# Performance work log

Hardware: AMD Instinct MI355X
Metric: run time of the kernel (lower is better)

## Reference

```python
import jax, jax.numpy as jnp
import numpy as np

N_NODES = 50000
N_EDGES = 800000
IN_DIM = 512
HEADS = 4
HID = 64
OUT = 64
NEG_SLOPE = 0.2  # DGL GATConv default


def gat_layer(x, W, attn_l, attn_r, bias, src, dst, n_nodes, heads, d_out):
    # x: [N, F_in], W: [F_in, heads*d_out], attn_l/attn_r: [heads, d_out], bias: [heads, d_out]
    f = (x @ W).reshape(n_nodes, heads, d_out)          # [N, H, D]
    el = jnp.sum(f * attn_l, axis=-1)                   # [N, H]
    er = jnp.sum(f * attn_r, axis=-1)                   # [N, H]
    e = jax.nn.leaky_relu(el[src] + er[dst], NEG_SLOPE) # [E, H]
    # segment softmax over incoming edges of each dst node
    m = jax.ops.segment_max(e, dst, num_segments=n_nodes)       # [N, H]
    ex = jnp.exp(e - m[dst])                                     # [E, H]
    den = jax.ops.segment_sum(ex, dst, num_segments=n_nodes)    # [N, H]
    a = ex / den[dst]                                            # [E, H]
    # scatter-aggregate weighted messages
    out = jax.ops.segment_sum(a[:, :, None] * f[src], dst, num_segments=n_nodes)  # [N, H, D]
    return out + bias, a


def setup_inputs() -> dict:
    key = jax.random.key(0)
    ks = jax.random.split(key, 12)
    features = jax.random.normal(ks[0], (N_NODES, IN_DIM), dtype=jnp.float32)
    src = jax.random.randint(ks[1], (N_EDGES,), 0, N_NODES, dtype=jnp.int32)
    dst = jax.random.randint(ks[2], (N_EDGES,), 0, N_NODES, dtype=jnp.int32)
    s1 = 1.0 / np.sqrt(IN_DIM)
    s2 = 1.0 / np.sqrt(HEADS * HID)
    W1 = jax.random.normal(ks[3], (IN_DIM, HEADS * HID), dtype=jnp.float32) * s1
    al1 = jax.random.normal(ks[4], (HEADS, HID), dtype=jnp.float32) * s1
    ar1 = jax.random.normal(ks[5], (HEADS, HID), dtype=jnp.float32) * s1
    b1 = jnp.zeros((HEADS, HID), dtype=jnp.float32)
    W2 = jax.random.normal(ks[6], (HEADS * HID, OUT), dtype=jnp.float32) * s2
    al2 = jax.random.normal(ks[7], (1, OUT), dtype=jnp.float32) * s2
    ar2 = jax.random.normal(ks[8], (1, OUT), dtype=jnp.float32) * s2
    b2 = jnp.zeros((1, OUT), dtype=jnp.float32)
    return {"features": features, "W1": W1, "al1": al1, "ar1": ar1, "b1": b1,
            "W2": W2, "al2": al2, "ar2": ar2, "b2": b2, "src": src, "dst": dst}


def reference(features, W1, al1, ar1, b1, W2, al2, ar2, b2, src, dst):
    h1, _ = gat_layer(features, W1, al1, ar1, b1, src, dst, N_NODES, HEADS, HID)
    h1 = jax.nn.elu(h1.reshape(N_NODES, HEADS * HID))   # flatten heads + ELU
    h2, _ = gat_layer(h1, W2, al2, ar2, b2, src, dst, N_NODES, 1, OUT)
    return h2  # [N, 1, OUT]
```

## Files before the change

### kernel.cpp

```cpp
#include <hip/hip_runtime.h>

#define N_NODES 50000
#define N_EDGES 800000
#define IN_DIM 512
#define NEG_SLOPE 0.2f

typedef short short8 __attribute__((ext_vector_type(8)));
typedef float f32x16 __attribute__((ext_vector_type(16)));

__device__ __forceinline__ unsigned bf16rne(float f) {
  union { float f; unsigned u; } v;
  v.f = f;
  return (v.u + 0x7FFFu + ((v.u >> 16) & 1u)) >> 16;
}
__device__ __forceinline__ float bf16tof(unsigned b) {
  union { unsigned u; float f; } v;
  v.u = b << 16;
  return v.f;
}
__device__ __forceinline__ void tsplit8(float4 a, float4 b, short8& hi,
                                        short8& lo) {
  float fa[8] = {a.x, a.y, a.z, a.w, b.x, b.y, b.z, b.w};
#pragma unroll
  for (int i = 0; i < 8; i++) {
    unsigned u = __float_as_uint(fa[i]);
    hi[i] = (short)(u >> 16);
    float lof = fa[i] - __uint_as_float(u & 0xffff0000u);
    lo[i] = (short)(__float_as_uint(lof) >> 16);
  }
}

__global__ void pack_w(const float* __restrict__ W, short* __restrict__ Bhi,
                       int N) {
  int k = blockIdx.x, n = threadIdx.x;
  float w = W[(size_t)k * N + n];
  int ksub = k >> 4, kh = (k >> 3) & 1, j = k & 7;
  int nsub = n >> 5, lane2 = (n & 31) | (kh << 5);
  size_t off = (((size_t)ksub * (N >> 5) + nsub) * 64 + lane2) * 8 + j;
  Bhi[off] = (short)bf16rne(w);
}

template <int K, int NSUBS, int NTILES>
__global__ __launch_bounds__(256) void gemm_mfma(
    const float* __restrict__ A, const short* __restrict__ Bhi_,
    unsigned short* __restrict__ Cb, const float* __restrict__ alv,
    const float* __restrict__ arv, float* __restrict__ el,
    float* __restrict__ er, int M) {
  const int N = NSUBS * 32;
  constexpr int U = 2;
  constexpr int G = K / 16 / U;
  int lane = threadIdx.x & 63;
  int wid = blockIdx.x * 4 + (threadIdx.x >> 6);
  int mtiles = (M + 31) >> 5;
  int mtile = wid / NTILES, ntile = wid % NTILES;
  if (mtile >= mtiles) return;
  int half = lane >> 5, l31 = lane & 31;
  int m0 = mtile * 32;
  int r0 = min(m0 + l31, M - 1);
  const float* ap = A + (size_t)r0 * K + half * 8;
  const short8* bh = (const short8*)Bhi_;
  size_t bidx = (size_t)(ntile * 2) * 64 + lane;
  f32x16 acc0 = {}, acc1 = {};
  float4 cx[U][2];
  short8 cb0[U], cb1[U];
#pragma unroll
  for (int u = 0; u < U; u++) {
    cx[u][0] = *(const float4*)(ap + u * 16);
    cx[u][1] = *(const float4*)(ap + u * 16 + 4);
    size_t bb = bidx + (size_t)u * NSUBS * 64;
    cb0[u] = bh[bb];
    cb1[u] = bh[bb + 64];
  }
  for (int g = 0; g < G; g++) {
    int gn = (g + 1 < G) ? g + 1 : g;
    float4 nx[U][2];
    short8 nb0[U], nb1[U];
#pragma unroll
    for (int u = 0; u < U; u++) {
      int ks = gn * U + u;
      nx[u][0] = *(const float4*)(ap + ks * 16);
      nx[u][1] = *(const float4*)(ap + ks * 16 + 4);
      size_t bb = bidx + (size_t)ks * NSUBS * 64;
      nb0[u] = bh[bb];
      nb1[u] = bh[bb + 64];
    }
#pragma unroll
    for (int u = 0; u < U; u++) {
      short8 ah, al8;
      tsplit8(cx[u][0], cx[u][1], ah, al8);
      acc0 = __builtin_amdgcn_mfma_f32_32x32x16_bf16(ah, cb0[u], acc0, 0, 0, 0);
      acc0 = __builtin_amdgcn_mfma_f32_32x32x16_bf16(al8, cb0[u], acc0, 0, 0, 0);
      acc1 = __builtin_amdgcn_mfma_f32_32x32x16_bf16(ah, cb1[u], acc1, 0, 0, 0);
      acc1 = __builtin_amdgcn_mfma_f32_32x32x16_bf16(al8, cb1[u], acc1, 0, 0, 0);
    }
#pragma unroll
    for (int u = 0; u < U; u++) {
      cx[u][0] = nx[u][0];
      cx[u][1] = nx[u][1];
      cb0[u] = nb0[u];
      cb1[u] = nb1[u];
    }
  }
  int colbase = ntile * 64 + l31;
  float wa0 = alv[colbase], wa1 = alv[colbase + 32];
  float wr0 = arv[colbase], wr1 = arv[colbase + 32];
#pragma unroll
  for (int r = 0; r < 16; r++) {
    int roff = (r & 3) + 8 * (r >> 2) + 4 * half;
    int row = m0 + roff;
    if (row < M) {
      Cb[(size_t)row * N + colbase] = (unsigned short)bf16rne(acc0[r]);
      Cb[(size_t)row * N + colbase + 32] = (unsigned short)bf16rne(acc1[r]);
    }
    float elv = acc0[r] * wa0 + acc1[r] * wa1;
    float erv = acc0[r] * wr0 + acc1[r] * wr1;
#pragma unroll
    for (int off = 1; off < 32; off <<= 1) {
      elv += __shfl_xor(elv, off);
      erv += __shfl_xor(erv, off);
    }
    if (l31 == 0 && row < M) {
      el[row * NTILES + ntile] = elv;
      er[row * NTILES + ntile] = erv;
    }
  }
}

__global__ void hist_kernel(const int* __restrict__ dst,
                            int* __restrict__ counts) {
  int e = blockIdx.x * blockDim.x + threadIdx.x;
  if (e < N_EDGES) atomicAdd(&counts[dst[e]], 1);
}

#define NSCAN 196
__global__ __launch_bounds__(256) void scan_part(const int* __restrict__ counts,
                                                 int* __restrict__ offsets,
                                                 int* __restrict__ bsums) {
  __shared__ int sh[256];
  int t = threadIdx.x;
  int i = blockIdx.x * 256 + t;
  int v = (i < N_NODES) ? counts[i] : 0;
  sh[t] = v;
  __syncthreads();
  for (int o = 1; o < 256; o <<= 1) {
    int x = (t >= o) ? sh[t - o] : 0;
    __syncthreads();
    sh[t] += x;
    __syncthreads();
  }
  if (i < N_NODES) offsets[i] = sh[t] - v;
  if (t == 255) bsums[blockIdx.x] = sh[255];
}
__global__ __launch_bounds__(256) void scan_top(int* __restrict__ bsums) {
  __shared__ int sh[256];
  int t = threadIdx.x;
  int v = (t < NSCAN) ? bsums[t] : 0;
  sh[t] = v;
  __syncthreads();
  for (int o = 1; o < 256; o <<= 1) {
    int x = (t >= o) ? sh[t - o] : 0;
    __syncthreads();
    sh[t] += x;
    __syncthreads();
  }
  if (t < NSCAN) bsums[t] = sh[t] - v;
}
__global__ __launch_bounds__(256) void scan_add(int* __restrict__ offsets,
                                                const int* __restrict__ bsums) {
  int i = blockIdx.x * 256 + threadIdx.x;
  if (i < N_NODES) offsets[i] += bsums[blockIdx.x];
  if (i == 0) offsets[N_NODES] = N_EDGES;
}

__global__ void scatter_kernel(const int* __restrict__ src,
                               const int* __restrict__ dst,
                               const int* __restrict__ offsets,
                               int* __restrict__ fill,
                               int* __restrict__ csr_src) {
  int e = blockIdx.x * blockDim.x + threadIdx.x;
  if (e < N_EDGES) {
    int d = dst[e];
    int pos = offsets[d] + atomicAdd(&fill[d], 1);
    csr_src[pos] = src[e];
  }
}

__global__ __launch_bounds__(256) void mden1_kernel(
    const int* __restrict__ offsets, const int* __restrict__ csr_src,
    const float* __restrict__ el, const float* __restrict__ er,
    float* __restrict__ mout, float* __restrict__ dout) {
  int w = threadIdx.x >> 6, lane = threadIdx.x & 63;
  int n = blockIdx.x * 4 + w;
  if (n >= N_NODES) return;
  int off0 = offsets[n], deg = offsets[n + 1] - off0;
  float4 erv = ((const float4*)er)[n];
  float er4[4] = {erv.x, erv.y, erv.z, erv.w};
  float m[4] = {-1e30f, -1e30f, -1e30f, -1e30f};
  float l[4] = {0.f, 0.f, 0.f, 0.f};
  for (int i = lane; i < deg; i += 64) {
    int s = csr_src[off0 + i];
    float4 elv = ((const float4*)el)[s];
    float e4[4] = {elv.x, elv.y, elv.z, elv.w};
#pragma unroll
    for (int h = 0; h < 4; h++) {
      float v = e4[h] + er4[h];
      v = v > 0.f ? v : NEG_SLOPE * v;
      float nm = fmaxf(m[h], v);
      l[h] = l[h] * __expf(m[h] - nm) + __expf(v - nm);
      m[h] = nm;
    }
  }
  for (int d = 32; d; d >>= 1) {
#pragma unroll
    for (int h = 0; h < 4; h++) {
      float mo = __shfl_down(m[h], d);
      float lo = __shfl_down(l[h], d);
      float nm = fmaxf(m[h], mo);
      l[h] = l[h] * __expf(m[h] - nm) + lo * __expf(mo - nm);
      m[h] = nm;
    }
  }
  if (lane == 0) {
#pragma unroll
    for (int h = 0; h < 4; h++) {
      mout[n * 4 + h] = m[h];
      dout[n * 4 + h] = l[h];
    }
  }
}

__global__ __launch_bounds__(256) void mden2_kernel(
    const int* __restrict__ offsets, const int* __restrict__ csr_src,
    const float* __restrict__ el, const float* __restrict__ er,
    float* __restrict__ mout, float* __restrict__ dout) {
  int w = threadIdx.x >> 6, lane = threadIdx.x & 63;
  int n = blockIdx.x * 4 + w;
  if (n >= N_NODES) return;
  int off0 = offsets[n], deg = offsets[n + 1] - off0;
  float ern = er[n];
  float m = -1e30f, l = 0.f;
  for (int i = lane; i < deg; i += 64) {
    int s = csr_src[off0 + i];
    float v = el[s] + ern;
    v = v > 0.f ? v : NEG_SLOPE * v;
    float nm = fmaxf(m, v);
    l = l * __expf(m - nm) + __expf(v - nm);
    m = nm;
  }
  for (int d = 32; d; d >>= 1) {
    float mo = __shfl_down(m, d);
    float lo = __shfl_down(l, d);
    float nm = fmaxf(m, mo);
    l = l * __expf(m - nm) + lo * __expf(mo - nm);
    m = nm;
  }
  if (lane == 0) {
    mout[n] = m;
    dout[n] = l;
  }
}

__global__ __launch_bounds__(256) void agg1_kernel(
    const int* __restrict__ offsets, const int* __restrict__ csr_src,
    const float* __restrict__ el, const float* __restrict__ er,
    const float* __restrict__ mm, const float* __restrict__ den,
    const unsigned short* __restrict__ fb, const float* __restrict__ bias,
    float* __restrict__ h1) {
  __shared__ float red[3][256];
  int n = blockIdx.x;
  int t = threadIdx.x;
  int w = t >> 6, lane = t & 63;
  int h = lane >> 4;
  int off0 = offsets[n], deg = offsets[n + 1] - off0;
  float erh = er[n * 4 + h];
  float mh = mm[n * 4 + h];
  float invd = 1.0f / den[n * 4 + h];
  float4 acc = {0.f, 0.f, 0.f, 0.f};
  float4 acc2 = {0.f, 0.f, 0.f, 0.f};
  int i = w;
  for (; i + 4 < deg; i += 8) {
    int s0 = csr_src[off0 + i];
    int s1 = csr_src[off0 + i + 4];
    float e0 = el[s0 * 4 + h] + erh;
    float e1 = el[s1 * 4 + h] + erh;
    e0 = e0 > 0.f ? e0 : NEG_SLOPE * e0;
    e1 = e1 > 0.f ? e1 : NEG_SLOPE * e1;
    float a0 = __expf(e0 - mh) * invd;
    float a1 = __expf(e1 - mh) * invd;
    uint2 p0 = *(const uint2*)(fb + (size_t)s0 * 256 + lane * 4);
    uint2 p1 = *(const uint2*)(fb + (size_t)s1 * 256 + lane * 4);
    acc.x += a0 * __uint_as_float(p0.x << 16);
    acc.y += a0 * __uint_as_float(p0.x & 0xffff0000u);
    acc.z += a0 * __uint_as_float(p0.y << 16);
    acc.w += a0 * __uint_as_float(p0.y & 0xffff0000u);
    acc2.x += a1 * __uint_as_float(p1.x << 16);
    acc2.y += a1 * __uint_as_float(p1.x & 0xffff0000u);
    acc2.z += a1 * __uint_as_float(p1.y << 16);
    acc2.w += a1 * __uint_as_float(p1.y & 0xffff0000u);
  }
  if (i < deg) {
    int s0 = csr_src[off0 + i];
    float e0 = el[s0 * 4 + h] + erh;
    e0 = e0 > 0.f ? e0 : NEG_SLOPE * e0;
    float a0 = __expf(e0 - mh) * invd;
    uint2 p0 = *(const uint2*)(fb + (size_t)s0 * 256 + lane * 4);
    acc.x += a0 * __uint_as_float(p0.x << 16);
    acc.y += a0 * __uint_as_float(p0.x & 0xffff0000u);
    acc.z += a0 * __uint_as_float(p0.y << 16);
    acc.w += a0 * __uint_as_float(p0.y & 0xffff0000u);
  }
  acc.x += acc2.x;
  acc.y += acc2.y;
  acc.z += acc2.z;
  acc.w += acc2.w;
  if (w) *(float4*)(&red[w - 1][lane * 4]) = acc;
  __syncthreads();
  if (w == 0) {
    float4 r0 = *(float4*)(&red[0][lane * 4]);
    float4 r1 = *(float4*)(&red[1][lane * 4]);
    float4 r2 = *(float4*)(&red[2][lane * 4]);
    float4 b = ((const float4*)bias)[lane];
    float o[4] = {acc.x + r0.x + r1.x + r2.x + b.x,
                  acc.y + r0.y + r1.y + r2.y + b.y,
                  acc.z + r0.z + r1.z + r2.z + b.z,
                  acc.w + r0.w + r1.w + r2.w + b.w};
#pragma unroll
    for (int j = 0; j < 4; j++) o[j] = o[j] > 0.f ? o[j] : __expf(o[j]) - 1.0f;
    float4 ov = {o[0], o[1], o[2], o[3]};
    *(float4*)(h1 + (size_t)n * 256 + lane * 4) = ov;
  }
}

__global__ __launch_bounds__(256) void agg2_kernel(
    const int* __restrict__ offsets, const int* __restrict__ csr_src,
    const float* __restrict__ el, const float* __restrict__ er,
    const float* __restrict__ mm, const float* __restrict__ den,
    const unsigned short* __restrict__ fb2, const float* __restrict__ bias,
    float* __restrict__ out) {
  int w = threadIdx.x >> 6, lane = threadIdx.x & 63;
  int n = blockIdx.x * 4 + w;
  if (n >= N_NODES) return;
  int dg = lane & 15, eslot = lane >> 4;
  int off0 = offsets[n], deg = offsets[n + 1] - off0;
  float ern = er[n], mn = mm[n];
  float invd = 1.0f / den[n];
  float4 acc = {0.f, 0.f, 0.f, 0.f};
  for (int i = eslot; i < deg; i += 4) {
    int s = csr_src[off0 + i];
    float e = el[s] + ern;
    e = e > 0.f ? e : NEG_SLOPE * e;
    float a = __expf(e - mn) * invd;
    uint2 p = *(const uint2*)(fb2 + (size_t)s * 64 + dg * 4);
    acc.x += a * __uint_as_float(p.x << 16);
    acc.y += a * __uint_as_float(p.x & 0xffff0000u);
    acc.z += a * __uint_as_float(p.y << 16);
    acc.w += a * __uint_as_float(p.y & 0xffff0000u);
  }
#pragma unroll
  for (int off = 16; off < 64; off <<= 1) {
    acc.x += __shfl_xor(acc.x, off);
    acc.y += __shfl_xor(acc.y, off);
    acc.z += __shfl_xor(acc.z, off);
    acc.w += __shfl_xor(acc.w, off);
  }
  if (eslot == 0) {
    float4 b = ((const float4*)bias)[dg];
    float4 ov = {acc.x + b.x, acc.y + b.y, acc.z + b.z, acc.w + b.w};
    *(float4*)(out + (size_t)n * 64 + dg * 4) = ov;
  }
}

extern "C" void kernel_launch(void* const* d_in, const int* in_sizes, int n_in,
                              void* d_out, int out_size, void* d_ws,
                              size_t ws_size, hipStream_t stream) {
  const float* features = (const float*)d_in[0];
  const float* W1 = (const float*)d_in[1];
  const float* al1 = (const float*)d_in[2];
  const float* ar1 = (const float*)d_in[3];
  const float* b1 = (const float*)d_in[4];
  const float* W2 = (const float*)d_in[5];
  const float* al2 = (const float*)d_in[6];
  const float* ar2 = (const float*)d_in[7];
  const float* b2 = (const float*)d_in[8];
  const int* src = (const int*)d_in[9];
  const int* dst = (const int*)d_in[10];
  float* out = (float*)d_out;

  float* h1 = (float*)d_ws;
  unsigned short* fb = (unsigned short*)(h1 + (size_t)N_NODES * 256);
  unsigned short* fb2 = fb;
  float* el1 = (float*)(fb + (size_t)N_NODES * 256);
  float* er1 = el1 + N_NODES * 4;
  float* m1 = er1 + N_NODES * 4;
  float* d1 = m1 + N_NODES * 4;
  float* el2 = d1 + N_NODES * 4;
  float* er2 = el2 + N_NODES;
  float* m2 = er2 + N_NODES;
  float* d2 = m2 + N_NODES;
  int* counts = (int*)(d2 + N_NODES);
  int* offsets = counts + N_NODES;
  int* fill = offsets + N_NODES + 1;
  int* csr_src = fill + N_NODES;
  int* bsums = csr_src + N_EDGES;

  short* b1hi = (short*)d_out;
  short* b2hi = (short*)fill;

  hipMemsetAsync(counts, 0, N_NODES * sizeof(int), stream);
  hipMemsetAsync(fill, 0, N_NODES * sizeof(int), stream);
  hist_kernel<<<(N_EDGES + 255) / 256, 256, 0, stream>>>(dst, counts);
  scan_part<<<NSCAN, 256, 0, stream>>>(counts, offsets, bsums);
  scan_top<<<1, 256, 0, stream>>>(bsums);
  scan_add<<<NSCAN, 256, 0, stream>>>(offsets, bsums);
  scatter_kernel<<<(N_EDGES + 255) / 256, 256, 0, stream>>>(src, dst, offsets,
                                                            fill, csr_src);

  pack_w<<<512, 256, 0, stream>>>(W1, b1hi, 256);
  pack_w<<<256, 64, 0, stream>>>(W2, b2hi, 64);

  gemm_mfma<IN_DIM, 8, 4><<<1563, 256, 0, stream>>>(features, b1hi, fb, al1,
                                                    ar1, el1, er1, N_NODES);
  mden1_kernel<<<(N_NODES + 3) / 4, 256, 0, stream>>>(offsets, csr_src, el1,
                                                      er1, m1, d1);
  agg1_kernel<<<N_NODES, 256, 0, stream>>>(offsets, csr_src, el1, er1, m1, d1,
                                           fb, b1, h1);

  gemm_mfma<256, 2, 1><<<391, 256, 0, stream>>>(h1, b2hi, fb2, al2, ar2, el2,
                                                er2, N_NODES);
  mden2_kernel<<<(N_NODES + 3) / 4, 256, 0, stream>>>(offsets, csr_src, el2,
                                                      er2, m2, d2);
  agg2_kernel<<<(N_NODES + 3) / 4, 256, 0, stream>>>(offsets, csr_src, el2, er2,
                                                     m2, d2, fb2, b2, out);
}
```

Baseline: 491.1 us.

## Stage GEMM A tiles through double-buffered LDS with direct global-to-LDS loads

Rewrites the MFMA GEMM so each block cooperatively loads 32-column A tiles into double-buffered shared memory using global_load_lds, with an XOR swizzle to avoid bank conflicts. Waves then read A fragments from LDS instead of each lane issuing strided global float4 loads. This reduces redundant global A traffic across the N-tiles and gives coalesced loads. In exchange it adds a block-wide barrier every K step and ties the block shape to the number of N-tiles.

```diff
diff --git a/kernel.cpp b/kernel.cpp
--- a/kernel.cpp
+++ b/kernel.cpp
@@ -7,6 +7,8 @@
 
 typedef short short8 __attribute__((ext_vector_type(8)));
 typedef float f32x16 __attribute__((ext_vector_type(16)));
+typedef __attribute__((address_space(3))) unsigned int lds_u32;
+typedef const __attribute__((address_space(1))) unsigned int glb_u32;
 
 __device__ __forceinline__ unsigned bf16rne(float f) {
   union { float f; unsigned u; } v;
@@ -46,68 +48,106 @@
     unsigned short* __restrict__ Cb, const float* __restrict__ alv,
     const float* __restrict__ arv, float* __restrict__ el,
     float* __restrict__ er, int M) {
-  const int N = NSUBS * 32;
-  constexpr int U = 2;
-  constexpr int G = K / 16 / U;
-  int lane = threadIdx.x & 63;
-  int wid = blockIdx.x * 4 + (threadIdx.x >> 6);
-  int mtiles = (M + 31) >> 5;
-  int mtile = wid / NTILES, ntile = wid % NTILES;
-  if (mtile >= mtiles) return;
-  int half = lane >> 5, l31 = lane & 31;
-  int m0 = mtile * 32;
-  int r0 = min(m0 + l31, M - 1);
-  const float* ap = A + (size_t)r0 * K + half * 8;
+  constexpr int N = NSUBS * 32;
+  constexpr int MT = 4 / NTILES;
+  constexpr int BROWS = MT * 32;
+  constexpr int T = K / 32;
+  __shared__ float ldsb[2][BROWS * 32];
+
+  const int tid = threadIdx.x;
+  const int lane = tid & 63;
+  const int w = tid >> 6;
+  const int l31 = lane & 31;
+  const int half = lane >> 5;
+  const int local_mt = w / NTILES;
+  const int ntile = w % NTILES;
+  const int block_row0 = blockIdx.x * BROWS;
+
+  const float* gsrc[MT];
+#pragma unroll
+  for (int q = 0; q < MT; q++) {
+    int seg = w * MT + q;
+    int r = seg * 8 + (lane >> 3);
+    int c = (lane & 7) ^ (r & 7);
+    int grow = block_row0 + r;
+    if (grow > M - 1) grow = M - 1;
+    gsrc[q] = A + (size_t)grow * K + c * 4;
+  }
+  unsigned lbase[MT];
+#pragma unroll
+  for (int q = 0; q < MT; q++) lbase[q] = (w * MT + q) * 256;
+
   const short8* bh = (const short8*)Bhi_;
-  size_t bidx = (size_t)(ntile * 2) * 64 + lane;
+  const size_t bbase = (size_t)(ntile * 2) * 64 + lane;
+
+  const int arow = local_mt * 32 + l31;
+  const int rs = arow & 7;
+
   f32x16 acc0 = {}, acc1 = {};
-  float4 cx[U][2];
-  short8 cb0[U], cb1[U];
-#pragma unroll
-  for (int u = 0; u < U; u++) {
-    cx[u][0] = *(const float4*)(ap + u * 16);
-    cx[u][1] = *(const float4*)(ap + u * 16 + 4);
-    size_t bb = bidx + (size_t)u * NSUBS * 64;
+  short8 cb0[2], cb1[2];
+
+#pragma unroll
+  for (int q = 0; q < MT; q++) {
+    __builtin_amdgcn_global_load_lds((glb_u32*)(gsrc[q]),
+                                     (lds_u32*)&ldsb[0][lbase[q]], 16, 0, 0);
+  }
+#pragma unroll
+  for (int u = 0; u < 2; u++) {
+    size_t bb = bbase + (size_t)u * NSUBS * 64;
     cb0[u] = bh[bb];
     cb1[u] = bh[bb + 64];
   }
-  for (int g = 0; g < G; g++) {
-    int gn = (g + 1 < G) ? g + 1 : g;
-    float4 nx[U][2];
-    short8 nb0[U], nb1[U];
-#pragma unroll
-    for (int u = 0; u < U; u++) {
-      int ks = gn * U + u;
-      nx[u][0] = *(const float4*)(ap + ks * 16);
-      nx[u][1] = *(const float4*)(ap + ks * 16 + 4);
-      size_t bb = bidx + (size_t)ks * NSUBS * 64;
+  __syncthreads();
+
+  int buf = 0;
+  for (int t = 0; t < T; t++) {
+    if (t + 1 < T) {
+      int kb = (t + 1) * 32;
+#pragma unroll
+      for (int q = 0; q < MT; q++) {
+        __builtin_amdgcn_global_load_lds((glb_u32*)(gsrc[q] + kb),
+                                         (lds_u32*)&ldsb[buf ^ 1][lbase[q]],
+                                         16, 0, 0);
+      }
+    }
+    int tn = (t + 1 < T) ? t + 1 : t;
+    short8 nb0[2], nb1[2];
+#pragma unroll
+    for (int u = 0; u < 2; u++) {
+      size_t bb = bbase + (size_t)(tn * 2 + u) * NSUBS * 64;
       nb0[u] = bh[bb];
       nb1[u] = bh[bb + 64];
     }
-#pragma unroll
-    for (int u = 0; u < U; u++) {
+    const float* lb = ldsb[buf];
+#pragma unroll
+    for (int u = 0; u < 2; u++) {
+      int c0 = u * 4 + half * 2;
+      float4 a0 = *(const float4*)&lb[arow * 32 + (c0 ^ rs) * 4];
+      float4 a1 = *(const float4*)&lb[arow * 32 + ((c0 + 1) ^ rs) * 4];
       short8 ah, al8;
-      tsplit8(cx[u][0], cx[u][1], ah, al8);
+      tsplit8(a0, a1, ah, al8);
       acc0 = __builtin_amdgcn_mfma_f32_32x32x16_bf16(ah, cb0[u], acc0, 0, 0, 0);
       acc0 = __builtin_amdgcn_mfma_f32_32x32x16_bf16(al8, cb0[u], acc0, 0, 0, 0);
       acc1 = __builtin_amdgcn_mfma_f32_32x32x16_bf16(ah, cb1[u], acc1, 0, 0, 0);
       acc1 = __builtin_amdgcn_mfma_f32_32x32x16_bf16(al8, cb1[u], acc1, 0, 0, 0);
     }
-#pragma unroll
-    for (int u = 0; u < U; u++) {
-      cx[u][0] = nx[u][0];
-      cx[u][1] = nx[u][1];
+    __syncthreads();
+#pragma unroll
+    for (int u = 0; u < 2; u++) {
       cb0[u] = nb0[u];
       cb1[u] = nb1[u];
     }
-  }
+    buf ^= 1;
+  }
+
   int colbase = ntile * 64 + l31;
   float wa0 = alv[colbase], wa1 = alv[colbase + 32];
   float wr0 = arv[colbase], wr1 = arv[colbase + 32];
+  const int mrow0 = block_row0 + local_mt * 32;
 #pragma unroll
   for (int r = 0; r < 16; r++) {
     int roff = (r & 3) + 8 * (r >> 2) + 4 * half;
-    int row = m0 + roff;
+    int row = mrow0 + roff;
     if (row < M) {
       Cb[(size_t)row * N + colbase] = (unsigned short)bf16rne(acc0[r]);
       Cb[(size_t)row * N + colbase + 32] = (unsigned short)bf16rne(acc1[r]);
```

Measured after the change: 466.4 us. 1.05x faster.
